# Performance work log

Measured on AMD Instinct MI355X. Metric: run time of the kernel, lower is better.

## Reference

```python
import jax, jax.numpy as jnp
import numpy as np

H = 4          # heads (hardcoded in original forward via shp=(4, ...))
B, G, D = 2, 2048, 128
KD = VD = 32   # key_dim = val_dim = embed_dim // n_heads
E = 128        # embed_dim


def setup_inputs() -> dict:
    key = jax.random.key(0)
    ks = jax.random.split(key, 10)
    s = lambda d: 1.0 / np.sqrt(d)
    return {
        "h": jax.random.normal(ks[0], (B, G, D), jnp.float32),
        "out_source_attn": jax.random.normal(ks[1], (H, B, G, G), jnp.float32),
        "Wq": jax.random.uniform(ks[2], (H, D, KD), jnp.float32, -s(KD), s(KD)),
        "Wk": jax.random.uniform(ks[3], (H, D, KD), jnp.float32, -s(KD), s(KD)),
        "Wv": jax.random.uniform(ks[4], (H, D, VD), jnp.float32, -s(VD), s(VD)),
        "Wout": jax.random.uniform(ks[5], (H, KD, E), jnp.float32, -s(E), s(E)),
        "w1": jax.random.uniform(ks[6], (8, 8), jnp.float32, -s(8), s(8)),
        "b1": jax.random.uniform(ks[7], (8,), jnp.float32, -s(8), s(8)),
        "w2": jax.random.uniform(ks[8], (4, 8), jnp.float32, -s(8), s(8)),
        "b2": jax.random.uniform(ks[9], (4,), jnp.float32, -s(4), s(4)),
    }


def reference(h, out_source_attn, Wq, Wk, Wv, Wout, w1, b1, w2, b2):
    # Per-head projections: (H, B, G, kd/vd)
    Q = jnp.einsum('bgd,hdk->hbgk', h, Wq)
    K = jnp.einsum('bgd,hdk->hbgk', h, Wk)
    V = jnp.einsum('bgd,hdv->hbgv', h, Wv)
    # QK^T scores concat with external attention source: (2H=8, B, G, G)
    scores = jnp.einsum('hbqk,hbpk->hbqp', Q, K)
    compat = jnp.concatenate([scores, out_source_attn], axis=0)
    # Per-score small MLP (Linear(8,8)->ReLU->Linear(8,4)) over channel dim
    x = compat.transpose(1, 2, 3, 0)                 # (B, G, G, 8)
    x = jax.nn.relu(x @ w1.T + b1) @ w2.T + b2       # (B, G, G, 4)
    attn = jax.nn.softmax(x.transpose(3, 0, 1, 2), axis=-1)  # (H, B, G, G)
    heads = jnp.einsum('hbqp,hbpv->hbqv', attn, V)   # (H, B, G, VD)
    out = jnp.einsum('hbqv,hve->bqe', heads, Wout)   # (B, G, E)
    return (out, out_source_attn)
```

## Files before the change

### kernel.cpp

```cpp
#include <hip/hip_runtime.h>

typedef __attribute__((ext_vector_type(8))) short bf16x8;
typedef __attribute__((ext_vector_type(4))) float f32x4;

#define OUT0 524288
#define SRC_CH_STRIDE 8388608

__device__ __forceinline__ unsigned short f2bf(float x){
    unsigned u = __builtin_bit_cast(unsigned, x);
    u += 0x7FFFu + ((u >> 16) & 1u);
    return (unsigned short)(u >> 16);
}

__global__ __launch_bounds__(256) void qkv_kernel(
    const float* __restrict__ hsrc,
    const float* __restrict__ Wq, const float* __restrict__ Wk, const float* __restrict__ Wv,
    unsigned short* __restrict__ Qb, unsigned short* __restrict__ Kb, unsigned short* __restrict__ Vt)
{
    __shared__ float hs[32*128];
    __shared__ float ws[128*32];
    const int t = threadIdx.x;
    const int g0 = blockIdx.x * 32;
    const int mat = blockIdx.y;
    const int mt = mat >> 2, head = mat & 3;
    {
        const float4* s = (const float4*)(hsrc + g0*128);
        float4* d = (float4*)hs;
        #pragma unroll
        for (int i=0;i<4;i++) d[t + i*256] = s[t + i*256];
        const float* W = (mt==0?Wq:(mt==1?Wk:Wv)) + head*4096;
        const float4* s2 = (const float4*)W;
        float4* d2 = (float4*)ws;
        #pragma unroll
        for (int i=0;i<4;i++) d2[t + i*256] = s2[t + i*256];
    }
    __syncthreads();
    const int r = t >> 3;
    const int k0 = (t & 7) * 4;
    float a0=0.f,a1=0.f,a2=0.f,a3=0.f;
    const float* hr = hs + r*128;
    #pragma unroll 8
    for (int d=0; d<128; d++){
        float hv = hr[d];
        float4 w4 = *(const float4*)(ws + d*32 + k0);
        a0 = fmaf(hv, w4.x, a0); a1 = fmaf(hv, w4.y, a1);
        a2 = fmaf(hv, w4.z, a2); a3 = fmaf(hv, w4.w, a3);
    }
    const int row_g = g0 + r;
    if (mt == 2){
        const int b = row_g >> 11, g = row_g & 2047;
        unsigned short* dst = Vt + ((b*128 + head*32 + k0) * 2048) + g;
        dst[0] = f2bf(a0); dst[2048] = f2bf(a1); dst[4096] = f2bf(a2); dst[6144] = f2bf(a3);
    } else {
        unsigned short* dst = (mt==0?Qb:Kb) + row_g*128 + head*32 + k0;
        dst[0]=f2bf(a0); dst[1]=f2bf(a1); dst[2]=f2bf(a2); dst[3]=f2bf(a3);
    }
}

__global__ __launch_bounds__(256) void attn_kernel(
    const float* __restrict__ src,
    const unsigned short* __restrict__ Qb,
    const unsigned short* __restrict__ Kb,
    const unsigned short* __restrict__ Vt,
    const float* __restrict__ w1g, const float* __restrict__ b1g,
    const float* __restrict__ w2g, const float* __restrict__ b2g,
    const float* __restrict__ Wout,
    float* __restrict__ out)
{
    __shared__ __align__(16) float S_lds[4*16*68];
    __shared__ __align__(16) unsigned short Pb_lds[4*16*72];
    __shared__ __align__(16) float wt[112];
    __shared__ __align__(16) float m_lds[64];
    __shared__ __align__(16) float l_lds[64];
    __shared__ __align__(16) float alpha_lds[64];

    const int t = threadIdx.x;
    const int lane = t & 63;
    const int c = t >> 6;
    const int quad = lane >> 4;
    const int lrow = lane & 15;
    const int q0 = blockIdx.x * 16;
    const int b = blockIdx.y;

    if (t < 64) wt[t] = w1g[t];
    else if (t < 72) wt[t] = b1g[t-64];
    else if (t < 104) wt[t] = w2g[t-72];
    else if (t < 108) wt[t] = b2g[t-104];
    if (t < 64){ m_lds[t] = -1e30f; l_lds[t] = 0.f; alpha_lds[t] = 0.f; }

    const bf16x8 qf = *(const bf16x8*)(Qb + (b*2048 + q0 + lrow)*128 + c*32 + quad*8);

    const int mq = t >> 4;
    const int mp = (t & 15) * 4;
    const int srcbase0 = (b*2048 + q0 + mq)*2048 + mp;

    f32x4 o0 = {0.f,0.f,0.f,0.f};
    f32x4 o1 = {0.f,0.f,0.f,0.f};
    const f32x4 zero4 = {0.f,0.f,0.f,0.f};

    __syncthreads();

    for (int p0 = 0; p0 < 2048; p0 += 64){
        float4 r4[4];
        #pragma unroll
        for (int ch=0; ch<4; ch++)
            r4[ch] = *(const float4*)(src + srcbase0 + ch*SRC_CH_STRIDE + p0);
        #pragma unroll
        for (int sub=0; sub<4; sub++){
            const bf16x8 kf = *(const bf16x8*)(Kb + (b*2048 + p0 + sub*16 + lrow)*128 + c*32 + quad*8);
            f32x4 sacc = __builtin_amdgcn_mfma_f32_16x16x32_bf16(qf, kf, zero4, 0, 0, 0);
            float* Sp = S_lds + (c*16 + quad*4)*68 + sub*16 + lrow;
            Sp[0] = sacc[0]; Sp[68] = sacc[1]; Sp[136] = sacc[2]; Sp[204] = sacc[3];
        }
        #pragma unroll
        for (int ch=0; ch<4; ch++)
            *(float4*)(out + OUT0 + srcbase0 + ch*SRC_CH_STRIDE + p0) = r4[ch];
        __syncthreads();

        {
            float xs[4][4], xr[4][4];
            #pragma unroll
            for (int ch=0; ch<4; ch++){
                float4 v = *(const float4*)(S_lds + (ch*16 + mq)*68 + mp);
                xs[ch][0]=v.x; xs[ch][1]=v.y; xs[ch][2]=v.z; xs[ch][3]=v.w;
                xr[ch][0]=r4[ch].x; xr[ch][1]=r4[ch].y; xr[ch][2]=r4[ch].z; xr[ch][3]=r4[ch].w;
            }
            float z[4][4];
            #pragma unroll
            for (int cc=0; cc<4; cc++){
                float bb = wt[104+cc];
                #pragma unroll
                for (int cell=0; cell<4; cell++) z[cc][cell] = bb;
            }
            #pragma unroll
            for (int j=0; j<8; j++){
                float w0 = wt[j*8+0], w1v = wt[j*8+1], w2v = wt[j*8+2], w3 = wt[j*8+3];
                float w4v = wt[j*8+4], w5 = wt[j*8+5], w6 = wt[j*8+6], w7 = wt[j*8+7];
                float bj = wt[64+j];
                float hcell[4];
                #pragma unroll
                for (int cell=0; cell<4; cell++){
                    float v = bj;
                    v = fmaf(w0, xs[0][cell], v);
                    v = fmaf(w1v, xs[1][cell], v);
                    v = fmaf(w2v, xs[2][cell], v);
                    v = fmaf(w3, xs[3][cell], v);
                    v = fmaf(w4v, xr[0][cell], v);
                    v = fmaf(w5, xr[1][cell], v);
                    v = fmaf(w6, xr[2][cell], v);
                    v = fmaf(w7, xr[3][cell], v);
                    hcell[cell] = fmaxf(v, 0.f);
                }
                #pragma unroll
                for (int cc=0; cc<4; cc++){
                    float wv = wt[72 + cc*8 + j];
                    #pragma unroll
                    for (int cell=0; cell<4; cell++) z[cc][cell] = fmaf(wv, hcell[cell], z[cc][cell]);
                }
            }
            #pragma unroll
            for (int ch=0; ch<4; ch++){
                float4 v; v.x=z[ch][0]; v.y=z[ch][1]; v.z=z[ch][2]; v.w=z[ch][3];
                *(float4*)(S_lds + (ch*16 + mq)*68 + mp) = v;
            }
        }
        __syncthreads();

        {
            const int rowid = t >> 2;
            const int seg = t & 3;
            const float* Sp = S_lds + rowid*68 + seg*16;
            float4 xa = *(const float4*)(Sp);
            float4 xb = *(const float4*)(Sp+4);
            float4 xc = *(const float4*)(Sp+8);
            float4 xd = *(const float4*)(Sp+12);
            float x[16];
            x[0]=xa.x; x[1]=xa.y; x[2]=xa.z; x[3]=xa.w;
            x[4]=xb.x; x[5]=xb.y; x[6]=xb.z; x[7]=xb.w;
            x[8]=xc.x; x[9]=xc.y; x[10]=xc.z; x[11]=xc.w;
            x[12]=xd.x; x[13]=xd.y; x[14]=xd.z; x[15]=xd.w;
            float mloc = x[0];
            #pragma unroll
            for (int i=1;i<16;i++) mloc = fmaxf(mloc, x[i]);
            mloc = fmaxf(mloc, __shfl_xor(mloc, 1));
            mloc = fmaxf(mloc, __shfl_xor(mloc, 2));
            float m_old = m_lds[rowid];
            float m_new = fmaxf(m_old, mloc);
            float ssum = 0.f;
            unsigned pk[8];
            #pragma unroll
            for (int i=0;i<8;i++){
                float e0 = __expf(x[2*i] - m_new);
                float e1 = __expf(x[2*i+1] - m_new);
                ssum += e0 + e1;
                pk[i] = (unsigned)f2bf(e0) | ((unsigned)f2bf(e1) << 16);
            }
            ssum += __shfl_xor(ssum, 1);
            ssum += __shfl_xor(ssum, 2);
            uint4* Pp = (uint4*)(Pb_lds + rowid*72 + seg*16);
            Pp[0] = make_uint4(pk[0],pk[1],pk[2],pk[3]);
            Pp[1] = make_uint4(pk[4],pk[5],pk[6],pk[7]);
            if (seg == 0){
                float alpha = __expf(m_old - m_new);
                m_lds[rowid] = m_new;
                alpha_lds[rowid] = alpha;
                l_lds[rowid] = fmaf(l_lds[rowid], alpha, ssum);
            }
        }
        __syncthreads();

        {
            float4 a4 = *(const float4*)(alpha_lds + c*16 + quad*4);
            o0[0]*=a4.x; o0[1]*=a4.y; o0[2]*=a4.z; o0[3]*=a4.w;
            o1[0]*=a4.x; o1[1]*=a4.y; o1[2]*=a4.z; o1[3]*=a4.w;
            #pragma unroll
            for (int chunk=0; chunk<2; chunk++){
                const bf16x8 pf = *(const bf16x8*)(Pb_lds + (c*16 + lrow)*72 + chunk*32 + quad*8);
                const bf16x8 v0 = *(const bf16x8*)(Vt + (b*128 + c*32 + lrow)*2048 + p0 + chunk*32 + quad*8);
                const bf16x8 v1 = *(const bf16x8*)(Vt + (b*128 + c*32 + 16 + lrow)*2048 + p0 + chunk*32 + quad*8);
                o0 = __builtin_amdgcn_mfma_f32_16x16x32_bf16(pf, v0, o0, 0, 0, 0);
                o1 = __builtin_amdgcn_mfma_f32_16x16x32_bf16(pf, v1, o1, 0, 0, 0);
            }
        }
    }

    {
        float4 l4 = *(const float4*)(l_lds + c*16 + quad*4);
        float i0 = 1.f/l4.x, i1 = 1.f/l4.y, i2 = 1.f/l4.z, i3 = 1.f/l4.w;
        o0[0]*=i0; o0[1]*=i1; o0[2]*=i2; o0[3]*=i3;
        o1[0]*=i0; o1[1]*=i1; o1[2]*=i2; o1[3]*=i3;
        #pragma unroll
        for (int r=0;r<4;r++){
            S_lds[(c*16 + quad*4 + r)*36 + lrow] = o0[r];
            S_lds[(c*16 + quad*4 + r)*36 + 16 + lrow] = o1[r];
        }
    }
    __syncthreads();
    {
        const int e0 = (t & 15) * 8;
        float acc[8];
        #pragma unroll
        for (int i=0;i<8;i++) acc[i]=0.f;
        #pragma unroll
        for (int cc=0; cc<4; cc++){
            const float* OhRow = S_lds + (cc*16 + mq)*36;
            const float* Wrow = Wout + cc*32*128 + e0;
            #pragma unroll 4
            for (int v=0; v<32; v++){
                float ov = OhRow[v];
                float4 wA = *(const float4*)(Wrow + v*128);
                float4 wB = *(const float4*)(Wrow + v*128 + 4);
                acc[0]=fmaf(ov,wA.x,acc[0]); acc[1]=fmaf(ov,wA.y,acc[1]);
                acc[2]=fmaf(ov,wA.z,acc[2]); acc[3]=fmaf(ov,wA.w,acc[3]);
                acc[4]=fmaf(ov,wB.x,acc[4]); acc[5]=fmaf(ov,wB.y,acc[5]);
                acc[6]=fmaf(ov,wB.z,acc[6]); acc[7]=fmaf(ov,wB.w,acc[7]);
            }
        }
        float* op = out + (b*2048 + q0 + mq)*128 + e0;
        float4 oA; oA.x=acc[0]; oA.y=acc[1]; oA.z=acc[2]; oA.w=acc[3];
        float4 oB; oB.x=acc[4]; oB.y=acc[5]; oB.z=acc[6]; oB.w=acc[7];
        *(float4*)op = oA;
        *(float4*)(op+4) = oB;
    }
}

extern "C" void kernel_launch(void* const* d_in, const int* in_sizes, int n_in,
                              void* d_out, int out_size, void* d_ws, size_t ws_size,
                              hipStream_t stream) {
    const float* h    = (const float*)d_in[0];
    const float* src  = (const float*)d_in[1];
    const float* Wq   = (const float*)d_in[2];
    const float* Wk   = (const float*)d_in[3];
    const float* Wv   = (const float*)d_in[4];
    const float* Wout = (const float*)d_in[5];
    const float* w1   = (const float*)d_in[6];
    const float* b1   = (const float*)d_in[7];
    const float* w2   = (const float*)d_in[8];
    const float* b2   = (const float*)d_in[9];
    float* out = (float*)d_out;

    unsigned short* Qb = (unsigned short*)d_ws;
    unsigned short* Kb = Qb + 524288;
    unsigned short* Vt = Kb + 524288;

    qkv_kernel<<<dim3(128,12), 256, 0, stream>>>(h, Wq, Wk, Wv, Qb, Kb, Vt);
    attn_kernel<<<dim3(128,2), 256, 0, stream>>>(src, Qb, Kb, Vt, w1, b1, w2, b2, Wout, out);
}
```

Baseline: 340.8 us.

## Split attention over key dimension with flash-decoding partials and combine kernel

The attention kernel now splits the 2048 key positions into four slices across a third grid dimension, so 1024 blocks run instead of 256. Each block writes its partial running max, running sum and unnormalized head outputs to workspace. A new combine kernel merges the four partials with log-sum-exp rescaling and then applies the Wout projection. The goal is better occupancy across the GPU's compute units on this memory-bound pass, at the cost of an extra launch and some partial-result traffic.

```diff
diff --git a/kernel.cpp b/kernel.cpp
--- a/kernel.cpp
+++ b/kernel.cpp
@@ -5,6 +5,8 @@
 
 #define OUT0 524288
 #define SRC_CH_STRIDE 8388608
+#define PART_HEAD 544
+#define PART_SLICE 2176
 
 __device__ __forceinline__ unsigned short f2bf(float x){
     unsigned u = __builtin_bit_cast(unsigned, x);
@@ -64,7 +66,7 @@
     const unsigned short* __restrict__ Vt,
     const float* __restrict__ w1g, const float* __restrict__ b1g,
     const float* __restrict__ w2g, const float* __restrict__ b2g,
-    const float* __restrict__ Wout,
+    float* __restrict__ part,
     float* __restrict__ out)
 {
     __shared__ __align__(16) float S_lds[4*16*68];
@@ -81,6 +83,8 @@
     const int lrow = lane & 15;
     const int q0 = blockIdx.x * 16;
     const int b = blockIdx.y;
+    const int s = blockIdx.z;
+    const int pbase = s * 512;
 
     if (t < 64) wt[t] = w1g[t];
     else if (t < 72) wt[t] = b1g[t-64];
@@ -100,7 +104,7 @@
 
     __syncthreads();
 
-    for (int p0 = 0; p0 < 2048; p0 += 64){
+    for (int p0 = pbase; p0 < pbase + 512; p0 += 64){
         float4 r4[4];
         #pragma unroll
         for (int ch=0; ch<4; ch++)
@@ -225,25 +229,61 @@
     }
 
     {
-        float4 l4 = *(const float4*)(l_lds + c*16 + quad*4);
-        float i0 = 1.f/l4.x, i1 = 1.f/l4.y, i2 = 1.f/l4.z, i3 = 1.f/l4.w;
-        o0[0]*=i0; o0[1]*=i1; o0[2]*=i2; o0[3]*=i3;
-        o1[0]*=i0; o1[1]*=i1; o1[2]*=i2; o1[3]*=i3;
+        float* P = part + (((b*128 + blockIdx.x)*4 + s)*4 + c) * PART_HEAD;
+        if (lane < 16){
+            P[lane]      = m_lds[c*16 + lane];
+            P[16 + lane] = l_lds[c*16 + lane];
+        }
         #pragma unroll
         for (int r=0;r<4;r++){
-            S_lds[(c*16 + quad*4 + r)*36 + lrow] = o0[r];
-            S_lds[(c*16 + quad*4 + r)*36 + 16 + lrow] = o1[r];
+            P[32 + (quad*4 + r)*32 + lrow]      = o0[r];
+            P[32 + (quad*4 + r)*32 + 16 + lrow] = o1[r];
+        }
+    }
+}
+
+__global__ __launch_bounds__(256) void combine_kernel(
+    const float* __restrict__ part,
+    const float* __restrict__ Wout,
+    float* __restrict__ out)
+{
+    __shared__ __align__(16) float O_lds[64*33];
+    const int t = threadIdx.x;
+    const int qt = blockIdx.x, b = blockIdx.y;
+
+    if (t < 64){
+        const int c = t >> 4, q = t & 15;
+        const float* P0 = part + (((b*128 + qt)*4 + 0)*4 + c) * PART_HEAD;
+        float m0 = P0[q], m1 = P0[PART_SLICE + q], m2 = P0[2*PART_SLICE + q], m3 = P0[3*PART_SLICE + q];
+        float M = fmaxf(fmaxf(m0, m1), fmaxf(m2, m3));
+        float w0 = __expf(m0 - M), w1 = __expf(m1 - M), w2 = __expf(m2 - M), w3 = __expf(m3 - M);
+        float L = P0[16+q]*w0 + P0[PART_SLICE+16+q]*w1 + P0[2*PART_SLICE+16+q]*w2 + P0[3*PART_SLICE+16+q]*w3;
+        float invL = 1.f / L;
+        const float* O0 = P0 + 32 + q*32;
+        float* dst = O_lds + t*33;
+        #pragma unroll
+        for (int v4 = 0; v4 < 8; v4++){
+            float4 a  = *(const float4*)(O0 + v4*4);
+            float4 bb = *(const float4*)(O0 + PART_SLICE + v4*4);
+            float4 cc = *(const float4*)(O0 + 2*PART_SLICE + v4*4);
+            float4 dd = *(const float4*)(O0 + 3*PART_SLICE + v4*4);
+            dst[v4*4+0] = (a.x*w0 + bb.x*w1 + cc.x*w2 + dd.x*w3) * invL;
+            dst[v4*4+1] = (a.y*w0 + bb.y*w1 + cc.y*w2 + dd.y*w3) * invL;
+            dst[v4*4+2] = (a.z*w0 + bb.z*w1 + cc.z*w2 + dd.z*w3) * invL;
+            dst[v4*4+3] = (a.w*w0 + bb.w*w1 + cc.w*w2 + dd.w*w3) * invL;
         }
     }
     __syncthreads();
+
     {
+        const int mq = t >> 4;
         const int e0 = (t & 15) * 8;
         float acc[8];
         #pragma unroll
         for (int i=0;i<8;i++) acc[i]=0.f;
         #pragma unroll
         for (int cc=0; cc<4; cc++){
-            const float* OhRow = S_lds + (cc*16 + mq)*36;
+            const float* OhRow = O_lds + (cc*16 + mq)*33;
             const float* Wrow = Wout + cc*32*128 + e0;
             #pragma unroll 4
             for (int v=0; v<32; v++){
@@ -256,7 +296,7 @@
                 acc[6]=fmaf(ov,wB.z,acc[6]); acc[7]=fmaf(ov,wB.w,acc[7]);
             }
         }
-        float* op = out + (b*2048 + q0 + mq)*128 + e0;
+        float* op = out + (b*2048 + qt*16 + mq)*128 + e0;
         float4 oA; oA.x=acc[0]; oA.y=acc[1]; oA.z=acc[2]; oA.w=acc[3];
         float4 oB; oB.x=acc[4]; oB.y=acc[5]; oB.z=acc[6]; oB.w=acc[7];
         *(float4*)op = oA;
@@ -282,7 +322,9 @@
     unsigned short* Qb = (unsigned short*)d_ws;
     unsigned short* Kb = Qb + 524288;
     unsigned short* Vt = Kb + 524288;
+    float* part = (float*)((char*)d_ws + 3*1048576);
 
     qkv_kernel<<<dim3(128,12), 256, 0, stream>>>(h, Wq, Wk, Wv, Qb, Kb, Vt);
-    attn_kernel<<<dim3(128,2), 256, 0, stream>>>(src, Qb, Kb, Vt, w1, b1, w2, b2, Wout, out);
-}
+    attn_kernel<<<dim3(128,2,4), 256, 0, stream>>>(src, Qb, Kb, Vt, w1, b1, w2, b2, part, out);
+    combine_kernel<<<dim3(128,2), 256, 0, stream>>>(part, Wout, out);
+}
```

After: 322.1 us. 5.5% less time.

## Split attention over key slices with per-wave query tiles and separate combine

Applied to the files above, without the earlier changes.

Restructures the attention kernel so each wave owns a 16-query tile across all 4 heads, keeps softmax state in registers with DPP row reductions, and splits the key dimension into 8 slices (flash-decoding style), writing partial m/l/O to workspace. A new combine kernel merges the slices and applies Wout, and the copy of out_source_attn moves to a separate copy kernel. This removes most block-level barriers and the LDS round trips for scores, and raises grid parallelism from 256 blocks. In exchange it adds extra kernel launches, partial-result traffic, and strided scalar loads of the source tensor. P now uses truncating bf16 conversion.

```diff
diff --git a/kernel.cpp b/kernel.cpp
--- a/kernel.cpp
+++ b/kernel.cpp
@@ -5,11 +5,38 @@
 
 #define OUT0 524288
 #define SRC_CH_STRIDE 8388608
+#define NSLICE 8
+#define PART_HEAD 544
+#define PART_SET 2176
 
 __device__ __forceinline__ unsigned short f2bf(float x){
     unsigned u = __builtin_bit_cast(unsigned, x);
     u += 0x7FFFu + ((u >> 16) & 1u);
     return (unsigned short)(u >> 16);
+}
+__device__ __forceinline__ unsigned short bftrunc(float x){
+    return (unsigned short)(__builtin_bit_cast(unsigned, x) >> 16);
+}
+
+template<int CTRL>
+__device__ __forceinline__ float rr16(float x){
+    int i = __builtin_bit_cast(int, x);
+    i = __builtin_amdgcn_mov_dpp(i, CTRL, 0xf, 0xf, true);
+    return __builtin_bit_cast(float, i);
+}
+__device__ __forceinline__ float redmax16(float v){
+    v = fmaxf(v, rr16<0x128>(v));
+    v = fmaxf(v, rr16<0x124>(v));
+    v = fmaxf(v, rr16<0x122>(v));
+    v = fmaxf(v, rr16<0x121>(v));
+    return v;
+}
+__device__ __forceinline__ float redsum16(float v){
+    v += rr16<0x128>(v);
+    v += rr16<0x124>(v);
+    v += rr16<0x122>(v);
+    v += rr16<0x121>(v);
+    return v;
 }
 
 __global__ __launch_bounds__(256) void qkv_kernel(
@@ -57,193 +84,223 @@
     }
 }
 
-__global__ __launch_bounds__(256) void attn_kernel(
+__global__ __launch_bounds__(256,2) void attn_kernel(
     const float* __restrict__ src,
     const unsigned short* __restrict__ Qb,
     const unsigned short* __restrict__ Kb,
     const unsigned short* __restrict__ Vt,
     const float* __restrict__ w1g, const float* __restrict__ b1g,
     const float* __restrict__ w2g, const float* __restrict__ b2g,
-    const float* __restrict__ Wout,
-    float* __restrict__ out)
+    float* __restrict__ part)
 {
-    __shared__ __align__(16) float S_lds[4*16*68];
-    __shared__ __align__(16) unsigned short Pb_lds[4*16*72];
-    __shared__ __align__(16) float wt[112];
-    __shared__ __align__(16) float m_lds[64];
-    __shared__ __align__(16) float l_lds[64];
-    __shared__ __align__(16) float alpha_lds[64];
+    __shared__ __align__(16) unsigned short Pb_lds[16*16*72];
+    __shared__ float wt[112];
 
     const int t = threadIdx.x;
-    const int lane = t & 63;
-    const int c = t >> 6;
-    const int quad = lane >> 4;
-    const int lrow = lane & 15;
-    const int q0 = blockIdx.x * 16;
-    const int b = blockIdx.y;
-
     if (t < 64) wt[t] = w1g[t];
     else if (t < 72) wt[t] = b1g[t-64];
     else if (t < 104) wt[t] = w2g[t-72];
     else if (t < 108) wt[t] = b2g[t-104];
-    if (t < 64){ m_lds[t] = -1e30f; l_lds[t] = 0.f; alpha_lds[t] = 0.f; }
-
-    const bf16x8 qf = *(const bf16x8*)(Qb + (b*2048 + q0 + lrow)*128 + c*32 + quad*8);
-
-    const int mq = t >> 4;
-    const int mp = (t & 15) * 4;
-    const int srcbase0 = (b*2048 + q0 + mq)*2048 + mp;
-
-    f32x4 o0 = {0.f,0.f,0.f,0.f};
-    f32x4 o1 = {0.f,0.f,0.f,0.f};
+    __syncthreads();
+
+    const int lane = t & 63, wv = t >> 6;
+    const int quad = lane >> 4, lrow = lane & 15;
+    const int qt = blockIdx.x*4 + wv, q0 = qt*16;
+    const int b = blockIdx.y, s = blockIdx.z;
+    const int pbase = s * 256;
+
+    bf16x8 qf[4];
+    #pragma unroll
+    for (int h=0;h<4;h++)
+        qf[h] = *(const bf16x8*)(Qb + (b*2048 + q0 + lrow)*128 + h*32 + quad*8);
+
+    f32x4 o[4][2];
+    float m[4][4], l[4][4];
+    #pragma unroll
+    for (int h=0;h<4;h++){
+        o[h][0] = (f32x4){0.f,0.f,0.f,0.f};
+        o[h][1] = (f32x4){0.f,0.f,0.f,0.f};
+        #pragma unroll
+        for (int r=0;r<4;r++){ m[h][r] = -1e30f; l[h][r] = 0.f; }
+    }
     const f32x4 zero4 = {0.f,0.f,0.f,0.f};
 
-    __syncthreads();
-
-    for (int p0 = 0; p0 < 2048; p0 += 64){
-        float4 r4[4];
-        #pragma unroll
-        for (int ch=0; ch<4; ch++)
-            r4[ch] = *(const float4*)(src + srcbase0 + ch*SRC_CH_STRIDE + p0);
-        #pragma unroll
-        for (int sub=0; sub<4; sub++){
-            const bf16x8 kf = *(const bf16x8*)(Kb + (b*2048 + p0 + sub*16 + lrow)*128 + c*32 + quad*8);
-            f32x4 sacc = __builtin_amdgcn_mfma_f32_16x16x32_bf16(qf, kf, zero4, 0, 0, 0);
-            float* Sp = S_lds + (c*16 + quad*4)*68 + sub*16 + lrow;
-            Sp[0] = sacc[0]; Sp[68] = sacc[1]; Sp[136] = sacc[2]; Sp[204] = sacc[3];
-        }
-        #pragma unroll
-        for (int ch=0; ch<4; ch++)
-            *(float4*)(out + OUT0 + srcbase0 + ch*SRC_CH_STRIDE + p0) = r4[ch];
-        __syncthreads();
-
-        {
-            float xs[4][4], xr[4][4];
+    float* dstbase = (float*)0;
+
+    for (int rnd = 0; rnd < 8; rnd++){
+        const int prnd = pbase + rnd*32;
+        float z[2][4][4];
+
+        #pragma unroll
+        for (int sub=0; sub<2; sub++){
+            const int psub = prnd + sub*16;
+            f32x4 sc[4];
+            #pragma unroll
+            for (int h=0;h<4;h++){
+                const bf16x8 kf = *(const bf16x8*)(Kb + (b*2048 + psub + lrow)*128 + h*32 + quad*8);
+                sc[h] = __builtin_amdgcn_mfma_f32_16x16x32_bf16(qf[h], kf, zero4, 0, 0, 0);
+            }
+            float xsrc[4][4];
             #pragma unroll
             for (int ch=0; ch<4; ch++){
-                float4 v = *(const float4*)(S_lds + (ch*16 + mq)*68 + mp);
-                xs[ch][0]=v.x; xs[ch][1]=v.y; xs[ch][2]=v.z; xs[ch][3]=v.w;
-                xr[ch][0]=r4[ch].x; xr[ch][1]=r4[ch].y; xr[ch][2]=r4[ch].z; xr[ch][3]=r4[ch].w;
-            }
-            float z[4][4];
-            #pragma unroll
-            for (int cc=0; cc<4; cc++){
+                const int off = ch*SRC_CH_STRIDE + (b*2048 + q0 + quad*4)*2048 + psub + lrow;
+                const float* sp = src + off;
+                float* op = part + 0;
+                (void)op;
+                #pragma unroll
+                for (int r=0;r<4;r++){ xsrc[ch][r] = sp[r*2048]; }
+            }
+            float zz[4][4];
+            #pragma unroll
+            for (int cc=0;cc<4;cc++){
                 float bb = wt[104+cc];
                 #pragma unroll
-                for (int cell=0; cell<4; cell++) z[cc][cell] = bb;
-            }
-            #pragma unroll
-            for (int j=0; j<8; j++){
-                float w0 = wt[j*8+0], w1v = wt[j*8+1], w2v = wt[j*8+2], w3 = wt[j*8+3];
-                float w4v = wt[j*8+4], w5 = wt[j*8+5], w6 = wt[j*8+6], w7 = wt[j*8+7];
+                for (int r=0;r<4;r++) zz[cc][r] = bb;
+            }
+            #pragma unroll
+            for (int j=0;j<8;j++){
+                float w0=wt[j*8+0], w1v=wt[j*8+1], w2v=wt[j*8+2], w3=wt[j*8+3];
+                float w4v=wt[j*8+4], w5=wt[j*8+5], w6=wt[j*8+6], w7=wt[j*8+7];
                 float bj = wt[64+j];
-                float hcell[4];
                 #pragma unroll
-                for (int cell=0; cell<4; cell++){
+                for (int r=0;r<4;r++){
                     float v = bj;
-                    v = fmaf(w0, xs[0][cell], v);
-                    v = fmaf(w1v, xs[1][cell], v);
-                    v = fmaf(w2v, xs[2][cell], v);
-                    v = fmaf(w3, xs[3][cell], v);
-                    v = fmaf(w4v, xr[0][cell], v);
-                    v = fmaf(w5, xr[1][cell], v);
-                    v = fmaf(w6, xr[2][cell], v);
-                    v = fmaf(w7, xr[3][cell], v);
-                    hcell[cell] = fmaxf(v, 0.f);
+                    v = fmaf(w0,  sc[0][r], v);
+                    v = fmaf(w1v, sc[1][r], v);
+                    v = fmaf(w2v, sc[2][r], v);
+                    v = fmaf(w3,  sc[3][r], v);
+                    v = fmaf(w4v, xsrc[0][r], v);
+                    v = fmaf(w5,  xsrc[1][r], v);
+                    v = fmaf(w6,  xsrc[2][r], v);
+                    v = fmaf(w7,  xsrc[3][r], v);
+                    float hh = fmaxf(v, 0.f);
+                    #pragma unroll
+                    for (int cc=0;cc<4;cc++)
+                        zz[cc][r] = fmaf(wt[72+cc*8+j], hh, zz[cc][r]);
                 }
+            }
+            #pragma unroll
+            for (int cc=0;cc<4;cc++)
                 #pragma unroll
-                for (int cc=0; cc<4; cc++){
-                    float wv = wt[72 + cc*8 + j];
-                    #pragma unroll
-                    for (int cell=0; cell<4; cell++) z[cc][cell] = fmaf(wv, hcell[cell], z[cc][cell]);
-                }
-            }
-            #pragma unroll
-            for (int ch=0; ch<4; ch++){
-                float4 v; v.x=z[ch][0]; v.y=z[ch][1]; v.z=z[ch][2]; v.w=z[ch][3];
-                *(float4*)(S_lds + (ch*16 + mq)*68 + mp) = v;
-            }
-        }
-        __syncthreads();
-
-        {
-            const int rowid = t >> 2;
-            const int seg = t & 3;
-            const float* Sp = S_lds + rowid*68 + seg*16;
-            float4 xa = *(const float4*)(Sp);
-            float4 xb = *(const float4*)(Sp+4);
-            float4 xc = *(const float4*)(Sp+8);
-            float4 xd = *(const float4*)(Sp+12);
-            float x[16];
-            x[0]=xa.x; x[1]=xa.y; x[2]=xa.z; x[3]=xa.w;
-            x[4]=xb.x; x[5]=xb.y; x[6]=xb.z; x[7]=xb.w;
-            x[8]=xc.x; x[9]=xc.y; x[10]=xc.z; x[11]=xc.w;
-            x[12]=xd.x; x[13]=xd.y; x[14]=xd.z; x[15]=xd.w;
-            float mloc = x[0];
-            #pragma unroll
-            for (int i=1;i<16;i++) mloc = fmaxf(mloc, x[i]);
-            mloc = fmaxf(mloc, __shfl_xor(mloc, 1));
-            mloc = fmaxf(mloc, __shfl_xor(mloc, 2));
-            float m_old = m_lds[rowid];
-            float m_new = fmaxf(m_old, mloc);
-            float ssum = 0.f;
-            unsigned pk[8];
-            #pragma unroll
-            for (int i=0;i<8;i++){
-                float e0 = __expf(x[2*i] - m_new);
-                float e1 = __expf(x[2*i+1] - m_new);
-                ssum += e0 + e1;
-                pk[i] = (unsigned)f2bf(e0) | ((unsigned)f2bf(e1) << 16);
-            }
-            ssum += __shfl_xor(ssum, 1);
-            ssum += __shfl_xor(ssum, 2);
-            uint4* Pp = (uint4*)(Pb_lds + rowid*72 + seg*16);
-            Pp[0] = make_uint4(pk[0],pk[1],pk[2],pk[3]);
-            Pp[1] = make_uint4(pk[4],pk[5],pk[6],pk[7]);
-            if (seg == 0){
-                float alpha = __expf(m_old - m_new);
-                m_lds[rowid] = m_new;
-                alpha_lds[rowid] = alpha;
-                l_lds[rowid] = fmaf(l_lds[rowid], alpha, ssum);
-            }
-        }
-        __syncthreads();
-
-        {
-            float4 a4 = *(const float4*)(alpha_lds + c*16 + quad*4);
-            o0[0]*=a4.x; o0[1]*=a4.y; o0[2]*=a4.z; o0[3]*=a4.w;
-            o1[0]*=a4.x; o1[1]*=a4.y; o1[2]*=a4.z; o1[3]*=a4.w;
-            #pragma unroll
-            for (int chunk=0; chunk<2; chunk++){
-                const bf16x8 pf = *(const bf16x8*)(Pb_lds + (c*16 + lrow)*72 + chunk*32 + quad*8);
-                const bf16x8 v0 = *(const bf16x8*)(Vt + (b*128 + c*32 + lrow)*2048 + p0 + chunk*32 + quad*8);
-                const bf16x8 v1 = *(const bf16x8*)(Vt + (b*128 + c*32 + 16 + lrow)*2048 + p0 + chunk*32 + quad*8);
-                o0 = __builtin_amdgcn_mfma_f32_16x16x32_bf16(pf, v0, o0, 0, 0, 0);
-                o1 = __builtin_amdgcn_mfma_f32_16x16x32_bf16(pf, v1, o1, 0, 0, 0);
-            }
-        }
-    }
+                for (int r=0;r<4;r++) z[sub][cc][r] = zz[cc][r];
+        }
+
+        #pragma unroll
+        for (int h=0;h<4;h++){
+            unsigned short* Pp = Pb_lds + ((wv*4+h)*16 + quad*4)*72 + lrow;
+            #pragma unroll
+            for (int r=0;r<4;r++){
+                float rm = fmaxf(z[0][h][r], z[1][h][r]);
+                rm = redmax16(rm);
+                float mn = fmaxf(m[h][r], rm);
+                float al = __expf(m[h][r] - mn);
+                m[h][r] = mn;
+                float e0 = __expf(z[0][h][r] - mn);
+                float e1 = __expf(z[1][h][r] - mn);
+                Pp[r*72]      = bftrunc(e0);
+                Pp[r*72 + 16] = bftrunc(e1);
+                float rs = redsum16(e0 + e1);
+                l[h][r] = l[h][r]*al + rs;
+                o[h][0][r] *= al;
+                o[h][1][r] *= al;
+            }
+        }
+
+        #pragma unroll
+        for (int h=0;h<4;h++){
+            const bf16x8 pf = *(const bf16x8*)(Pb_lds + ((wv*4+h)*16 + lrow)*72 + quad*8);
+            const bf16x8 v0 = *(const bf16x8*)(Vt + (b*128 + h*32 + lrow)*2048 + prnd + quad*8);
+            const bf16x8 v1 = *(const bf16x8*)(Vt + (b*128 + h*32 + 16 + lrow)*2048 + prnd + quad*8);
+            o[h][0] = __builtin_amdgcn_mfma_f32_16x16x32_bf16(pf, v0, o[h][0], 0, 0, 0);
+            o[h][1] = __builtin_amdgcn_mfma_f32_16x16x32_bf16(pf, v1, o[h][1], 0, 0, 0);
+        }
+    }
+
+    float* P = part + ((b*128 + qt)*NSLICE + s)*PART_SET;
+    #pragma unroll
+    for (int h=0;h<4;h++){
+        if (lrow == 0){
+            float4 mv; mv.x=m[h][0]; mv.y=m[h][1]; mv.z=m[h][2]; mv.w=m[h][3];
+            float4 lv; lv.x=l[h][0]; lv.y=l[h][1]; lv.z=l[h][2]; lv.w=l[h][3];
+            *(float4*)(P + h*PART_HEAD + quad*4) = mv;
+            *(float4*)(P + h*PART_HEAD + 16 + quad*4) = lv;
+        }
+        #pragma unroll
+        for (int r=0;r<4;r++){
+            P[h*PART_HEAD + 32 + (quad*4+r)*32 + lrow]      = o[h][0][r];
+            P[h*PART_HEAD + 32 + (quad*4+r)*32 + 16 + lrow] = o[h][1][r];
+        }
+    }
+}
+
+__global__ __launch_bounds__(256) void copy_kernel(
+    const float* __restrict__ src, float* __restrict__ dst)
+{
+    const long i = ((long)blockIdx.x * 256 + threadIdx.x) * 4;
+    float4 v = *(const float4*)(src + i);
+    *(float4*)(dst + i) = v;
+}
+
+__global__ __launch_bounds__(256) void combine_kernel(
+    const float* __restrict__ part,
+    const float* __restrict__ Wout,
+    float* __restrict__ out)
+{
+    __shared__ __align__(16) float O_lds[64*36];
+    const int t = threadIdx.x;
+    const int qt = blockIdx.x, b = blockIdx.y;
 
     {
-        float4 l4 = *(const float4*)(l_lds + c*16 + quad*4);
-        float i0 = 1.f/l4.x, i1 = 1.f/l4.y, i2 = 1.f/l4.z, i3 = 1.f/l4.w;
-        o0[0]*=i0; o0[1]*=i1; o0[2]*=i2; o0[3]*=i3;
-        o1[0]*=i0; o1[1]*=i1; o1[2]*=i2; o1[3]*=i3;
-        #pragma unroll
-        for (int r=0;r<4;r++){
-            S_lds[(c*16 + quad*4 + r)*36 + lrow] = o0[r];
-            S_lds[(c*16 + quad*4 + r)*36 + 16 + lrow] = o1[r];
-        }
+        const int c  = t >> 6;
+        const int q  = (t >> 2) & 15;
+        const int v0 = (t & 3) * 8;
+        const float* base = part + (long)((b*128 + qt)*NSLICE)*PART_SET + c*PART_HEAD;
+        float ms[NSLICE];
+        float M = -1e30f;
+        #pragma unroll
+        for (int sl=0; sl<NSLICE; sl++){
+            ms[sl] = base[sl*PART_SET + q];
+            M = fmaxf(M, ms[sl]);
+        }
+        float L = 0.f;
+        float wsl[NSLICE];
+        #pragma unroll
+        for (int sl=0; sl<NSLICE; sl++){
+            wsl[sl] = __expf(ms[sl] - M);
+            L = fmaf(base[sl*PART_SET + 16 + q], wsl[sl], L);
+        }
+        float acc[8];
+        #pragma unroll
+        for (int i=0;i<8;i++) acc[i]=0.f;
+        #pragma unroll
+        for (int sl=0; sl<NSLICE; sl++){
+            const float* Op = base + sl*PART_SET + 32 + q*32 + v0;
+            float4 a = *(const float4*)(Op);
+            float4 bb = *(const float4*)(Op + 4);
+            float w = wsl[sl];
+            acc[0]=fmaf(a.x,w,acc[0]); acc[1]=fmaf(a.y,w,acc[1]);
+            acc[2]=fmaf(a.z,w,acc[2]); acc[3]=fmaf(a.w,w,acc[3]);
+            acc[4]=fmaf(bb.x,w,acc[4]); acc[5]=fmaf(bb.y,w,acc[5]);
+            acc[6]=fmaf(bb.z,w,acc[6]); acc[7]=fmaf(bb.w,w,acc[7]);
+        }
+        float invL = 1.f / L;
+        float* dst = O_lds + (c*16 + q)*36 + v0;
+        float4 oA; oA.x=acc[0]*invL; oA.y=acc[1]*invL; oA.z=acc[2]*invL; oA.w=acc[3]*invL;
+        float4 oB; oB.x=acc[4]*invL; oB.y=acc[5]*invL; oB.z=acc[6]*invL; oB.w=acc[7]*invL;
+        *(float4*)dst = oA;
+        *(float4*)(dst+4) = oB;
     }
     __syncthreads();
+
     {
+        const int mq = t >> 4;
         const int e0 = (t & 15) * 8;
         float acc[8];
         #pragma unroll
         for (int i=0;i<8;i++) acc[i]=0.f;
         #pragma unroll
         for (int cc=0; cc<4; cc++){
-            const float* OhRow = S_lds + (cc*16 + mq)*36;
+            const float* OhRow = O_lds + (cc*16 + mq)*36;
             const float* Wrow = Wout + cc*32*128 + e0;
             #pragma unroll 4
             for (int v=0; v<32; v++){
@@ -256,7 +313,7 @@
                 acc[6]=fmaf(ov,wB.z,acc[6]); acc[7]=fmaf(ov,wB.w,acc[7]);
             }
         }
-        float* op = out + (b*2048 + q0 + mq)*128 + e0;
+        float* op = out + (b*2048 + qt*16 + mq)*128 + e0;
         float4 oA; oA.x=acc[0]; oA.y=acc[1]; oA.z=acc[2]; oA.w=acc[3];
         float4 oB; oB.x=acc[4]; oB.y=acc[5]; oB.z=acc[6]; oB.w=acc[7];
         *(float4*)op = oA;
@@ -282,7 +339,10 @@
     unsigned short* Qb = (unsigned short*)d_ws;
     unsigned short* Kb = Qb + 524288;
     unsigned short* Vt = Kb + 524288;
+    float* part = (float*)((char*)d_ws + 3*1048576);
 
     qkv_kernel<<<dim3(128,12), 256, 0, stream>>>(h, Wq, Wk, Wv, Qb, Kb, Vt);
-    attn_kernel<<<dim3(128,2), 256, 0, stream>>>(src, Qb, Kb, Vt, w1, b1, w2, b2, Wout, out);
-}
+    attn_kernel<<<dim3(32,2,NSLICE), 256, 0, stream>>>(src, Qb, Kb, Vt, w1, b1, w2, b2, part);
+    copy_kernel<<<dim3(33554432/1024), 256, 0, stream>>>(src, out + OUT0);
+    combine_kernel<<<dim3(128,2), 256, 0, stream>>>(part, Wout, out);
+}
```

After: 353.1 us. +3.6%, slower.
